# Kernel optimization log

Measured on AMD Instinct MI355X. Metric: run time of the kernel, lower is better.

## Reference

```python
import jax, jax.numpy as jnp
import numpy as np

B, S, D, H = 4, 2048, 1024, 16
HD = D // H  # head_dim = 64
SCALE = HD ** -0.5


def setup_inputs() -> dict:
    key = jax.random.key(0)
    k1, k2, k3, k4, k5 = jax.random.split(key, 5)
    std = D ** -0.5
    return {
        "x": jax.random.normal(k1, (B, S, D), dtype=jnp.float32),
        "w_qkv": jax.random.normal(k2, (D, 3 * D), dtype=jnp.float32) * std,
        "b_qkv": jax.random.normal(k3, (3 * D,), dtype=jnp.float32) * 0.01,
        "w_out": jax.random.normal(k4, (D, D), dtype=jnp.float32) * std,
        "b_out": jax.random.normal(k5, (D,), dtype=jnp.float32) * 0.01,
    }


def reference(x, w_qkv, b_qkv, w_out, b_out):
    b, s, d = x.shape
    qkv = x @ w_qkv + b_qkv                                   # [B,S,3D]
    qkv = qkv.reshape(b, s, 3, H, HD).transpose(2, 0, 3, 1, 4)  # [3,B,H,S,HD]
    q, k, v = qkv[0], qkv[1], qkv[2]
    attn = jnp.einsum("bhqd,bhkd->bhqk", q, k) * SCALE        # [B,H,S,S]
    attn = jax.nn.softmax(attn, axis=-1)
    out = jnp.einsum("bhqk,bhkd->bhqd", attn, v)              # [B,H,S,HD]
    out = out.transpose(0, 2, 1, 3).reshape(b, s, d)          # [B,S,D]
    return out @ w_out + b_out
```

## Files before the change

### kernel.cpp

```cpp
#include <hip/hip_runtime.h>
#include <stdint.h>
#include <stddef.h>

#define NB 4
#define NS 2048
#define ND 1024
#define NH 16
#define HDIM 64
#define SCALE 0.125f

typedef __attribute__((ext_vector_type(4))) float f32x4;
typedef __attribute__((ext_vector_type(16))) float f32x16;
typedef __attribute__((ext_vector_type(8))) __bf16 bf16x8;
typedef __attribute__((ext_vector_type(4))) uint32_t u32x4;

__device__ __forceinline__ uint16_t f2bf(float f) {
  uint32_t u = __builtin_bit_cast(uint32_t, f);
  return (uint16_t)((u + 0x7fffu + ((u >> 16) & 1u)) >> 16);
}

__device__ __forceinline__ void gload_lds16(const void* g, void* l) {
  __builtin_amdgcn_global_load_lds((const __attribute__((address_space(1))) void*)g,
                                   (__attribute__((address_space(3))) void*)l, 16, 0, 0);
}

__device__ __forceinline__ uint32_t cvtpk(float lo, float hi) {
  uint32_t r;
  asm("v_cvt_pk_bf16_f32 %0, %1, %2" : "=v"(r) : "v"(lo), "v"(hi));
  return r;
}

__device__ __forceinline__ void permswap(uint32_t& a, uint32_t& b) {
  asm("v_permlane32_swap_b32 %0, %1" : "+v"(a), "+v"(b));
}

__device__ __forceinline__ float fexp2(float x) {
  float r;
  asm("v_exp_f32 %0, %1" : "=v"(r) : "v"(x));
  return r;
}

__global__ void k_cvt_bf16(const float* __restrict__ in, uint16_t* __restrict__ out, int n4) {
  int i = blockIdx.x * blockDim.x + threadIdx.x;
  if (i >= n4) return;
  float4 v = reinterpret_cast<const float4*>(in)[i];
  ushort4 o;
  o.x = f2bf(v.x); o.y = f2bf(v.y); o.z = f2bf(v.z); o.w = f2bf(v.w);
  reinterpret_cast<ushort4*>(out)[i] = o;
}

__global__ void k_transpose_cvt(const float* __restrict__ in, uint16_t* __restrict__ out,
                                int K, int N) {
  __shared__ float tile[64][65];
  const int nb = blockIdx.x * 64, kb = blockIdx.y * 64;
  const int c = threadIdx.x & 63, r0 = threadIdx.x >> 6;
#pragma unroll
  for (int i = 0; i < 16; ++i) {
    int r = r0 * 16 + i;
    tile[r][c] = in[(size_t)(kb + r) * N + nb + c];
  }
  __syncthreads();
#pragma unroll
  for (int i = 0; i < 16; ++i) {
    int rr = r0 * 16 + i;
    out[(size_t)(nb + rr) * K + kb + c] = f2bf(tile[c][rr]);
  }
}

__global__ void k_vt_repack(const uint16_t* __restrict__ qkv, uint16_t* __restrict__ vt) {
  __shared__ uint16_t tile[64][66];
  const int bh = blockIdx.y, sb = blockIdx.x * 64;
  const int b = bh >> 4, h = bh & 15;
  const int c = threadIdx.x & 63, r0 = threadIdx.x >> 6;
#pragma unroll
  for (int i = 0; i < 16; ++i) {
    int s = r0 * 16 + i;
    tile[s][c] = qkv[(size_t)(b * NS + sb + s) * 3072 + 2048 + h * 64 + c];
  }
  __syncthreads();
#pragma unroll
  for (int i = 0; i < 16; ++i) {
    int d = r0 * 16 + i;
    vt[(size_t)bh * 64 * NS + (size_t)d * NS + sb + c] = tile[c][d];
  }
}

__global__ __launch_bounds__(512)
void k_gemm256(const uint16_t* __restrict__ A, const uint16_t* __restrict__ Bt,
               const float* __restrict__ bias, uint16_t* __restrict__ C,
               int M, int N, int K) {
  __shared__ __align__(16) char Al[3][32768];
  __shared__ __align__(16) char Bl[3][16384];
  const int tid = threadIdx.x, wave = tid >> 6, lane = tid & 63;

  const int flat = blockIdx.y * gridDim.x + blockIdx.x;
  const int cpx = (gridDim.x * gridDim.y) >> 3;
  const int swz = (flat & 7) * cpx + (flat >> 3);
  const int bx = swz % gridDim.x, by = swz / gridDim.x;
  const int mb = by * 256, nb = bx * 128;

  const int wm = wave >> 1, wn = wave & 1;
  const int fr = lane & 15, cc = lane >> 4;
  f32x4 acc[4][4] = {};
  const int NT = K >> 6;
  const int sslot = tid & 7;

#define STAGE(BUF, KT) do {                                                     \
    const int kb_ = (KT) * 64;                                                  \
    _Pragma("unroll")                                                           \
    for (int i = 0; i < 4; ++i) {                                               \
      int row = (i * 512 + tid) >> 3;                                           \
      int ch = sslot ^ (row & 7);                                               \
      gload_lds16(A + (size_t)(mb + row) * K + kb_ + ch * 8,                    \
                  Al[BUF] + (size_t)(i * 512 + (wave << 6)) * 16);              \
    }                                                                           \
    _Pragma("unroll")                                                           \
    for (int i = 0; i < 2; ++i) {                                               \
      int row = (i * 512 + tid) >> 3;                                           \
      int ch = sslot ^ (row & 7);                                               \
      gload_lds16(Bt + (size_t)(nb + row) * K + kb_ + ch * 8,                   \
                  Bl[BUF] + (size_t)(i * 512 + (wave << 6)) * 16);              \
    }                                                                           \
  } while (0)

  STAGE(0, 0);
  STAGE(1, 1);
  asm volatile("s_waitcnt vmcnt(6)" ::: "memory");
  __builtin_amdgcn_s_barrier();

  int cur = 0;
  for (int kt = 0; kt < NT; ++kt) {
    const bool issue = (kt + 2 < NT);
    if (issue) STAGE((kt + 2) % 3, kt + 2);

#pragma unroll
    for (int ks = 0; ks < 2; ++ks) {
      bf16x8 af[4], bfg[4];
#pragma unroll
      for (int i = 0; i < 4; ++i) {
        int ra = wm * 64 + i * 16 + fr;
        af[i] = *(const bf16x8*)(Al[cur] + ra * 128 + (((ks * 4 + cc) ^ (ra & 7)) * 16));
        int rb = wn * 64 + i * 16 + fr;
        bfg[i] = *(const bf16x8*)(Bl[cur] + rb * 128 + (((ks * 4 + cc) ^ (rb & 7)) * 16));
      }
      __builtin_amdgcn_s_setprio(1);
#pragma unroll
      for (int i = 0; i < 4; ++i)
#pragma unroll
        for (int j = 0; j < 4; ++j)
          acc[i][j] = __builtin_amdgcn_mfma_f32_16x16x32_bf16(af[i], bfg[j], acc[i][j], 0, 0, 0);
      __builtin_amdgcn_s_setprio(0);
    }

    if (kt + 1 < NT) {
      if (issue) asm volatile("s_waitcnt vmcnt(6)" ::: "memory");
      else       asm volatile("s_waitcnt vmcnt(0)" ::: "memory");
      __builtin_amdgcn_s_barrier();
    }
    cur = (cur + 1) % 3;
  }
#undef STAGE

#pragma unroll
  for (int i = 0; i < 4; ++i)
#pragma unroll
    for (int j = 0; j < 4; ++j)
#pragma unroll
      for (int r = 0; r < 4; ++r) {
        int row = mb + wm * 64 + i * 16 + cc * 4 + r;
        int col = nb + wn * 64 + j * 16 + fr;
        C[(size_t)row * N + col] = f2bf(acc[i][j][r] + bias[col]);
      }
}

template<int OUT_BF16>
__global__ __launch_bounds__(256)
void k_gemm(const uint16_t* __restrict__ A, const uint16_t* __restrict__ Bt,
            const float* __restrict__ bias, void* __restrict__ C,
            int M, int N, int K) {
  __shared__ __align__(16) char Al[8192];
  __shared__ __align__(16) char Bl[8192];
  const int tid = threadIdx.x;
  const int wave = tid >> 6, lane = tid & 63;
  const int mb = blockIdx.y * 128, nb = blockIdx.x * 128;
  const int wm = (wave >> 1) * 64, wn = (wave & 1) * 64;
  const int fr = lane & 15, cc = lane >> 4;
  const int srow = tid >> 2, sch = tid & 3;
  f32x4 acc[4][4] = {};

  for (int kb = 0; kb < K; kb += 32) {
#pragma unroll
    for (int p = 0; p < 2; ++p) {
      int row = p * 64 + srow;
      int cg = sch ^ (row & 3) ^ ((row >> 2) & 3);
      gload_lds16(A + (size_t)(mb + row) * K + kb + cg * 8, Al + p * 4096 + wave * 1024);
      gload_lds16(Bt + (size_t)(nb + row) * K + kb + cg * 8, Bl + p * 4096 + wave * 1024);
    }
    __syncthreads();
    bf16x8 af[4], bfr[4];
#pragma unroll
    for (int i = 0; i < 4; ++i) {
      int ra = wm + i * 16 + fr;
      af[i] = *(const bf16x8*)(Al + ra * 64 + ((cc ^ (ra & 3) ^ ((ra >> 2) & 3)) * 16));
      int rb = wn + i * 16 + fr;
      bfr[i] = *(const bf16x8*)(Bl + rb * 64 + ((cc ^ (rb & 3) ^ ((rb >> 2) & 3)) * 16));
    }
#pragma unroll
    for (int i = 0; i < 4; ++i)
#pragma unroll
      for (int j = 0; j < 4; ++j)
        acc[i][j] = __builtin_amdgcn_mfma_f32_16x16x32_bf16(af[i], bfr[j], acc[i][j], 0, 0, 0);
    __syncthreads();
  }

#pragma unroll
  for (int i = 0; i < 4; ++i)
#pragma unroll
    for (int j = 0; j < 4; ++j)
#pragma unroll
      for (int r = 0; r < 4; ++r) {
        int row = mb + wm + i * 16 + cc * 4 + r;
        int col = nb + wn + j * 16 + fr;
        float v = acc[i][j][r] + bias[col];
        if (OUT_BF16)
          ((uint16_t*)C)[(size_t)row * N + col] = f2bf(v);
        else
          ((float*)C)[(size_t)row * N + col] = v;
      }
}

__global__ __launch_bounds__(256)
void k_attn(const uint16_t* __restrict__ qkv, const uint16_t* __restrict__ vt,
            uint16_t* __restrict__ out) {
  __shared__ __align__(16) char Kl[2][8192];
  __shared__ __align__(16) char Vl[2][8192];

  const int id = blockIdx.y * 16 + blockIdx.x;
  const int wfid = (id & 7) * 128 + (id >> 3);
  const int bh = wfid >> 4, qblk = wfid & 15;
  const int b = bh >> 4, h = bh & 15;
  const int tid = threadIdx.x, wave = tid >> 6, lane = tid & 63;
  const int ln31 = lane & 31, hi = lane >> 5;

  const int q0 = qblk * 128 + wave * 32;
  const uint16_t* qrowp = qkv + (size_t)(b * NS + q0 + ln31) * 3072 + h * 64 + hi * 8;
  bf16x8 qf[4];
#pragma unroll
  for (int kk = 0; kk < 4; ++kk) qf[kk] = *(const bf16x8*)(qrowp + kk * 16);

  const int srow = tid >> 3;
  const int cs = (tid & 7) ^ (srow & 7);
  const uint16_t* ksrc = qkv + (size_t)(b * NS) * 3072 + 1024 + h * 64 + cs * 8;
  const uint16_t* vsrc = vt + (size_t)bh * 64 * NS + cs * 8;

  f32x16 acc0 = {}, acc1 = {};
  float m_run = -1e30f, l_run = 0.f;
  const float C = 0.18033688011112042f;

#pragma unroll
  for (int r = 0; r < 2; ++r) {
    int row = srow + r * 32;
    gload_lds16(ksrc + (size_t)row * 3072, Kl[0] + wave * 1024 + r * 4096);
    gload_lds16(vsrc + (size_t)row * NS, Vl[0] + wave * 1024 + r * 4096);
  }
  __syncthreads();

  const int ksw = ln31 & 7;

  for (int t = 0; t < NS / 64; ++t) {
    const int cur = t & 1;
    if (t < NS / 64 - 1) {
      const int kb2 = (t + 1) * 64;
      char* kd = Kl[cur ^ 1] + wave * 1024;
      char* vd = Vl[cur ^ 1] + wave * 1024;
#pragma unroll
      for (int r = 0; r < 2; ++r) {
        int row = srow + r * 32;
        gload_lds16(ksrc + (size_t)(kb2 + row) * 3072, kd + r * 4096);
        gload_lds16(vsrc + (size_t)row * NS + kb2, vd + r * 4096);
      }
    }

    const char* kb0 = Kl[cur] + ln31 * 128;
    const char* kb1 = kb0 + 32 * 128;
    f32x16 st0 = {}, st1 = {};
    __builtin_amdgcn_s_setprio(1);
#pragma unroll
    for (int kk = 0; kk < 4; ++kk) {
      int c = ((kk * 2 + hi) ^ ksw) * 16;
      bf16x8 k0 = *(const bf16x8*)(kb0 + c);
      bf16x8 k1 = *(const bf16x8*)(kb1 + c);
      st0 = __builtin_amdgcn_mfma_f32_32x32x16_bf16(k0, qf[kk], st0, 0, 0, 0);
      st1 = __builtin_amdgcn_mfma_f32_32x32x16_bf16(k1, qf[kk], st1, 0, 0, 0);
    }
    __builtin_amdgcn_s_setprio(0);

    float mx = st0[0];
#pragma unroll
    for (int r = 1; r < 16; ++r) mx = fmaxf(mx, st0[r]);
#pragma unroll
    for (int r = 0; r < 16; ++r) mx = fmaxf(mx, st1[r]);
    mx = fmaxf(mx, __shfl_xor(mx, 32));
    if (__ballot(mx > m_run + 64.f)) {
      float mn = fmaxf(m_run, mx);
      float al = fexp2((m_run - mn) * C);
      m_run = mn; l_run *= al;
#pragma unroll
      for (int r = 0; r < 16; ++r) { acc0[r] *= al; acc1[r] *= al; }
    }
    const float nmc = -m_run * C;
    float rs = 0.f;
#pragma unroll
    for (int r = 0; r < 16; ++r) { st0[r] = fexp2(fmaf(st0[r], C, nmc)); rs += st0[r]; }
#pragma unroll
    for (int r = 0; r < 16; ++r) { st1[r] = fexp2(fmaf(st1[r], C, nmc)); rs += st1[r]; }
    rs += __shfl_xor(rs, 32);
    l_run += rs;

    const char* vb0 = Vl[cur] + ln31 * 128;
    const char* vb1 = vb0 + 32 * 128;
    __builtin_amdgcn_s_setprio(1);
#pragma unroll
    for (int h2 = 0; h2 < 2; ++h2) {
      f32x16 ph = h2 ? st1 : st0;
#pragma unroll
      for (int s2 = 0; s2 < 2; ++s2) {
        const int kkp = h2 * 2 + s2;
        const int s8 = s2 * 8;
        uint32_t A0 = cvtpk(ph[s8 + 0], ph[s8 + 1]);
        uint32_t A1 = cvtpk(ph[s8 + 2], ph[s8 + 3]);
        uint32_t B0 = cvtpk(ph[s8 + 4], ph[s8 + 5]);
        uint32_t B1 = cvtpk(ph[s8 + 6], ph[s8 + 7]);
        permswap(A0, B0);
        permswap(A1, B1);
        u32x4 pw = {A0, A1, B0, B1};
        bf16x8 pf = __builtin_bit_cast(bf16x8, pw);
        int c = ((kkp * 2 + hi) ^ ksw) * 16;
        bf16x8 v0 = *(const bf16x8*)(vb0 + c);
        bf16x8 v1 = *(const bf16x8*)(vb1 + c);
        acc0 = __builtin_amdgcn_mfma_f32_32x32x16_bf16(v0, pf, acc0, 0, 0, 0);
        acc1 = __builtin_amdgcn_mfma_f32_32x32x16_bf16(v1, pf, acc1, 0, 0, 0);
      }
    }
    __builtin_amdgcn_s_setprio(0);

    __syncthreads();
  }

  const float rl = 1.0f / l_run;
  char* sc = (char*)Kl + wave * 4096 + ln31 * 128;
  const int qsw = ln31 & 15;
#pragma unroll
  for (int dn = 0; dn < 2; ++dn) {
    f32x16 a = dn ? acc1 : acc0;
#pragma unroll
    for (int g = 0; g < 4; ++g) {
      uint2 w;
      w.x = cvtpk(a[4 * g + 0] * rl, a[4 * g + 1] * rl);
      w.y = cvtpk(a[4 * g + 2] * rl, a[4 * g + 3] * rl);
      int c8 = (dn * 8 + 2 * g + hi) ^ qsw;
      *(uint2*)(sc + c8 * 8) = w;
    }
  }
  char* outp = (char*)out + ((size_t)(b * NS + q0 + ln31) * 1024 + h * 64 + hi * 32) * 2;
#pragma unroll
  for (int cc2 = 0; cc2 < 4; ++cc2) {
    uint2 va = *(const uint2*)(sc + (((hi * 8 + 2 * cc2 + 0) ^ qsw) * 8));
    uint2 vb2 = *(const uint2*)(sc + (((hi * 8 + 2 * cc2 + 1) ^ qsw) * 8));
    u32x4 o = {va.x, va.y, vb2.x, vb2.y};
    *(u32x4*)(outp + cc2 * 16) = o;
  }
}

extern "C" void kernel_launch(void* const* d_in, const int* in_sizes, int n_in,
                              void* d_out, int out_size, void* d_ws, size_t ws_size,
                              hipStream_t stream) {
  const float* x     = (const float*)d_in[0];
  const float* w_qkv = (const float*)d_in[1];
  const float* b_qkv = (const float*)d_in[2];
  const float* w_out = (const float*)d_in[3];
  const float* b_out = (const float*)d_in[4];
  float* out = (float*)d_out;
  char* ws = (char*)d_ws;

  uint16_t* Xb    = (uint16_t*)(ws);
  uint16_t* Wqkvt = (uint16_t*)(ws + (16u << 20));
  uint16_t* Woutt = (uint16_t*)(ws + (22u << 20));
  uint16_t* QKV   = (uint16_t*)(ws + (24u << 20));
  uint16_t* Vt    = (uint16_t*)(ws + (72u << 20));
  uint16_t* AO    = Xb;

  k_cvt_bf16<<<(NB * NS * ND / 4 + 255) / 256, 256, 0, stream>>>(x, Xb, NB * NS * ND / 4);
  k_transpose_cvt<<<dim3(48, 16), 256, 0, stream>>>(w_qkv, Wqkvt, ND, 3 * ND);
  k_transpose_cvt<<<dim3(16, 16), 256, 0, stream>>>(w_out, Woutt, ND, ND);
  k_gemm256<<<dim3(24, 32), 512, 0, stream>>>(Xb, Wqkvt, b_qkv, QKV, NB * NS, 3 * ND, ND);
  k_vt_repack<<<dim3(32, 64), 256, 0, stream>>>(QKV, Vt);
  k_attn<<<dim3(16, 64), 256, 0, stream>>>(QKV, Vt, AO);
  k_gemm<0><<<dim3(8, 64), 256, 0, stream>>>(AO, Woutt, b_out, out, NB * NS, ND, ND);
}
```

Measured before the change: 229.7 us.

## Fuse prep kernels, write V transposed from QKV GEMM, split attention launch

Merges the x conversion and both weight transpose-conversions into one launch. The QKV GEMM epilogue now writes the V columns straight into the transposed Vt layout, which removes the separate repack kernel and its extra read and write of V. The attention launch is split into two half-grids, the max reduction becomes a tree, and the cross-half row-sum shuffle is deferred to the end. The Vt writes are strided 8-byte stores, and the second attention launch adds launch overhead.

Result: no change. 226.6 us (-1.3%).

```diff
diff --git a/kernel.cpp b/kernel.cpp
--- a/kernel.cpp
+++ b/kernel.cpp
@@ -40,20 +40,25 @@
   return r;
 }
 
-__global__ void k_cvt_bf16(const float* __restrict__ in, uint16_t* __restrict__ out, int n4) {
-  int i = blockIdx.x * blockDim.x + threadIdx.x;
-  if (i >= n4) return;
-  float4 v = reinterpret_cast<const float4*>(in)[i];
-  ushort4 o;
-  o.x = f2bf(v.x); o.y = f2bf(v.y); o.z = f2bf(v.z); o.w = f2bf(v.w);
-  reinterpret_cast<ushort4*>(out)[i] = o;
-}
-
-__global__ void k_transpose_cvt(const float* __restrict__ in, uint16_t* __restrict__ out,
-                                int K, int N) {
+__global__ __launch_bounds__(256)
+void k_prep(const float* __restrict__ x, const float* __restrict__ wq,
+            const float* __restrict__ wo, uint16_t* __restrict__ Xb,
+            uint16_t* __restrict__ Wq, uint16_t* __restrict__ Wo) {
   __shared__ float tile[64][65];
-  const int nb = blockIdx.x * 64, kb = blockIdx.y * 64;
-  const int c = threadIdx.x & 63, r0 = threadIdx.x >> 6;
+  const int bid = blockIdx.x, tid = threadIdx.x;
+  if (bid < 8192) {
+    int i = bid * 256 + tid;
+    float4 v = reinterpret_cast<const float4*>(x)[i];
+    ushort4 o;
+    o.x = f2bf(v.x); o.y = f2bf(v.y); o.z = f2bf(v.z); o.w = f2bf(v.w);
+    reinterpret_cast<ushort4*>(Xb)[i] = o;
+    return;
+  }
+  const float* in; uint16_t* out; int K, N, bx, by;
+  if (bid < 8960) { int r = bid - 8192; in = wq; out = Wq; K = 1024; N = 3072; bx = r % 48; by = r / 48; }
+  else            { int r = bid - 8960; in = wo; out = Wo; K = 1024; N = 1024; bx = r % 16; by = r / 16; }
+  const int nb = bx * 64, kb = by * 64;
+  const int c = tid & 63, r0 = tid >> 6;
 #pragma unroll
   for (int i = 0; i < 16; ++i) {
     int r = r0 * 16 + i;
@@ -67,28 +72,10 @@
   }
 }
 
-__global__ void k_vt_repack(const uint16_t* __restrict__ qkv, uint16_t* __restrict__ vt) {
-  __shared__ uint16_t tile[64][66];
-  const int bh = blockIdx.y, sb = blockIdx.x * 64;
-  const int b = bh >> 4, h = bh & 15;
-  const int c = threadIdx.x & 63, r0 = threadIdx.x >> 6;
-#pragma unroll
-  for (int i = 0; i < 16; ++i) {
-    int s = r0 * 16 + i;
-    tile[s][c] = qkv[(size_t)(b * NS + sb + s) * 3072 + 2048 + h * 64 + c];
-  }
-  __syncthreads();
-#pragma unroll
-  for (int i = 0; i < 16; ++i) {
-    int d = r0 * 16 + i;
-    vt[(size_t)bh * 64 * NS + (size_t)d * NS + sb + c] = tile[c][d];
-  }
-}
-
 __global__ __launch_bounds__(512)
 void k_gemm256(const uint16_t* __restrict__ A, const uint16_t* __restrict__ Bt,
                const float* __restrict__ bias, uint16_t* __restrict__ C,
-               int M, int N, int K) {
+               uint16_t* __restrict__ vt, int M, int N, int K) {
   __shared__ __align__(16) char Al[3][32768];
   __shared__ __align__(16) char Bl[3][16384];
   const int tid = threadIdx.x, wave = tid >> 6, lane = tid & 63;
@@ -161,16 +148,38 @@
   }
 #undef STAGE
 
-#pragma unroll
-  for (int i = 0; i < 4; ++i)
-#pragma unroll
-    for (int j = 0; j < 4; ++j)
-#pragma unroll
-      for (int r = 0; r < 4; ++r) {
-        int row = mb + wm * 64 + i * 16 + cc * 4 + r;
+  if (nb < 2048) {
+#pragma unroll
+    for (int i = 0; i < 4; ++i)
+#pragma unroll
+      for (int j = 0; j < 4; ++j)
+#pragma unroll
+        for (int r = 0; r < 4; ++r) {
+          int row = mb + wm * 64 + i * 16 + cc * 4 + r;
+          int col = nb + wn * 64 + j * 16 + fr;
+          C[(size_t)row * N + col] = f2bf(acc[i][j][r] + bias[col]);
+        }
+  } else {
+    const int b_ = mb >> 11;
+    const int h_ = ((nb - 2048) >> 6) + wn;
+    const int s0 = (mb & 2047) + wm * 64;
+    uint16_t* vb = vt + (size_t)(b_ * 16 + h_) * 64 * NS;
+#pragma unroll
+    for (int i = 0; i < 4; ++i)
+#pragma unroll
+      for (int j = 0; j < 4; ++j) {
         int col = nb + wn * 64 + j * 16 + fr;
-        C[(size_t)row * N + col] = f2bf(acc[i][j][r] + bias[col]);
+        int d = j * 16 + fr;
+        float bcol = bias[col];
+        ushort4 o;
+        o.x = f2bf(acc[i][j][0] + bcol);
+        o.y = f2bf(acc[i][j][1] + bcol);
+        o.z = f2bf(acc[i][j][2] + bcol);
+        o.w = f2bf(acc[i][j][3] + bcol);
+        int s = s0 + i * 16 + cc * 4;
+        *reinterpret_cast<ushort4*>(vb + (size_t)d * NS + s) = o;
       }
+  }
 }
 
 template<int OUT_BF16>
@@ -231,13 +240,13 @@
 
 __global__ __launch_bounds__(256)
 void k_attn(const uint16_t* __restrict__ qkv, const uint16_t* __restrict__ vt,
-            uint16_t* __restrict__ out) {
+            uint16_t* __restrict__ out, int bh0) {
   __shared__ __align__(16) char Kl[2][8192];
   __shared__ __align__(16) char Vl[2][8192];
 
   const int id = blockIdx.y * 16 + blockIdx.x;
-  const int wfid = (id & 7) * 128 + (id >> 3);
-  const int bh = wfid >> 4, qblk = wfid & 15;
+  const int wfid = (id & 7) * 64 + (id >> 3);
+  const int bh = bh0 + (wfid >> 4), qblk = wfid & 15;
   const int b = bh >> 4, h = bh & 15;
   const int tid = threadIdx.x, wave = tid >> 6, lane = tid & 63;
   const int ln31 = lane & 31, hi = lane >> 5;
@@ -295,11 +304,12 @@
     }
     __builtin_amdgcn_s_setprio(0);
 
-    float mx = st0[0];
-#pragma unroll
-    for (int r = 1; r < 16; ++r) mx = fmaxf(mx, st0[r]);
-#pragma unroll
-    for (int r = 0; r < 16; ++r) mx = fmaxf(mx, st1[r]);
+    float t8[8];
+#pragma unroll
+    for (int r = 0; r < 8; ++r)
+      t8[r] = fmaxf(fmaxf(st0[r], st0[r + 8]), fmaxf(st1[r], st1[r + 8]));
+    float mx = fmaxf(fmaxf(fmaxf(t8[0], t8[1]), fmaxf(t8[2], t8[3])),
+                     fmaxf(fmaxf(t8[4], t8[5]), fmaxf(t8[6], t8[7])));
     mx = fmaxf(mx, __shfl_xor(mx, 32));
     if (__ballot(mx > m_run + 64.f)) {
       float mn = fmaxf(m_run, mx);
@@ -314,7 +324,6 @@
     for (int r = 0; r < 16; ++r) { st0[r] = fexp2(fmaf(st0[r], C, nmc)); rs += st0[r]; }
 #pragma unroll
     for (int r = 0; r < 16; ++r) { st1[r] = fexp2(fmaf(st1[r], C, nmc)); rs += st1[r]; }
-    rs += __shfl_xor(rs, 32);
     l_run += rs;
 
     const char* vb0 = Vl[cur] + ln31 * 128;
@@ -347,7 +356,7 @@
     __syncthreads();
   }
 
-  const float rl = 1.0f / l_run;
+  const float rl = 1.0f / (l_run + __shfl_xor(l_run, 32));
   char* sc = (char*)Kl + wave * 4096 + ln31 * 128;
   const int qsw = ln31 & 15;
 #pragma unroll
@@ -390,11 +399,9 @@
   uint16_t* Vt    = (uint16_t*)(ws + (72u << 20));
   uint16_t* AO    = Xb;
 
-  k_cvt_bf16<<<(NB * NS * ND / 4 + 255) / 256, 256, 0, stream>>>(x, Xb, NB * NS * ND / 4);
-  k_transpose_cvt<<<dim3(48, 16), 256, 0, stream>>>(w_qkv, Wqkvt, ND, 3 * ND);
-  k_transpose_cvt<<<dim3(16, 16), 256, 0, stream>>>(w_out, Woutt, ND, ND);
-  k_gemm256<<<dim3(24, 32), 512, 0, stream>>>(Xb, Wqkvt, b_qkv, QKV, NB * NS, 3 * ND, ND);
-  k_vt_repack<<<dim3(32, 64), 256, 0, stream>>>(QKV, Vt);
-  k_attn<<<dim3(16, 64), 256, 0, stream>>>(QKV, Vt, AO);
+  k_prep<<<9216, 256, 0, stream>>>(x, w_qkv, w_out, Xb, Wqkvt, Woutt);
+  k_gemm256<<<dim3(24, 32), 512, 0, stream>>>(Xb, Wqkvt, b_qkv, QKV, Vt, NB * NS, 3 * ND, ND);
+  k_attn<<<dim3(16, 32), 256, 0, stream>>>(QKV, Vt, AO, 0);
+  k_attn<<<dim3(16, 32), 256, 0, stream>>>(QKV, Vt, AO, 32);
   k_gemm<0><<<dim3(8, 64), 256, 0, stream>>>(AO, Woutt, b_out, out, NB * NS, ND, ND);
 }
```
